# Kernel tuning notes

Measured on AMD Instinct MI355X. Metric: run time of the kernel, lower is better.

The kernel has to match this reference:

```python
import jax, jax.numpy as jnp
import numpy as np

D_MODEL = 1024
N_HEAD = 16


def setup_inputs() -> dict:
    key = jax.random.key(0)
    ks = jax.random.split(key, 12)
    B, T, D = 2, 2048, D_MODEL
    s = 1.0 / np.sqrt(D)
    return {
        "q": jax.random.normal(ks[0], (B, T, D), jnp.float32),
        "k": jax.random.normal(ks[1], (B, T, D), jnp.float32),
        "v": jax.random.normal(ks[2], (B, T, D), jnp.float32),
        "w_q": jax.random.normal(ks[3], (D, D), jnp.float32) * s,
        "b_q": jnp.zeros((D,), jnp.float32),
        "w_k": jax.random.normal(ks[4], (D, D), jnp.float32) * s,
        "b_k": jnp.zeros((D,), jnp.float32),
        "w_v": jax.random.normal(ks[5], (D, D), jnp.float32) * s,
        "b_v": jnp.zeros((D,), jnp.float32),
        "w_o": jax.random.normal(ks[6], (D, D), jnp.float32) * s,
        "b_o": jnp.zeros((D,), jnp.float32),
    }


def reference(q, k, v, w_q, b_q, w_k, b_k, w_v, b_v, w_o, b_o):
    B, T, D = q.shape
    H = N_HEAD
    nd = D // H  # head dim
    # projections (weights stored as [in, out])
    qh = (q @ w_q + b_q).reshape(B, T, H, nd).transpose(0, 2, 1, 3)  # [b,h,t,nd]
    kh = (k @ w_k + b_k).reshape(B, T, H, nd).transpose(0, 2, 1, 3)
    vh = (v @ w_v + b_v).reshape(B, T, H, nd).transpose(0, 2, 1, 3)
    score = jnp.einsum('bhqd,bhkd->bhqk', qh, kh) / jnp.sqrt(jnp.float32(nd))
    causal = jnp.tril(jnp.ones((T, T), dtype=bool))  # [tq, tk]
    score = jnp.where(causal, score, -jnp.inf)
    # NOTE: original module uses nn.Softmax(dim=-2), i.e. softmax over the
    # QUERY axis. Faithful to the source.
    attn = jax.nn.softmax(score, axis=-2)
    out = jnp.einsum('bhqk,bhkd->bhqd', attn, vh)  # [b,h,t,nd]
    out = out.transpose(0, 2, 1, 3).reshape(B, T, D)
    return out @ w_o + b_o
```

## Files before the change

### kernel.cpp

```cpp
#include <hip/hip_runtime.h>
#include <hip/hip_bf16.h>
#include <cstdint>
#include <cstddef>

#define D_MODEL 1024
#define NHEAD   16
#define HDIM    64
#define BB      2
#define TT      2048
#define MM      (BB*TT)
#define BHN     (BB*NHEAD)

typedef __attribute__((ext_vector_type(8))) __bf16 bf16x8;
typedef __attribute__((ext_vector_type(4))) float  f32x4;
typedef __attribute__((ext_vector_type(8))) unsigned short u16x8;
typedef __attribute__((ext_vector_type(4))) unsigned short u16x4;

__device__ __forceinline__ unsigned short f2b(float f){
  __bf16 b = (__bf16)f;
  return __builtin_bit_cast(unsigned short, b);
}

__device__ __forceinline__ f32x4 mfma16(bf16x8 a, bf16x8 b, f32x4 c){
  return __builtin_amdgcn_mfma_f32_16x16x32_bf16(a, b, c, 0, 0, 0);
}

__device__ __forceinline__ void gload16(const void* g, void* lds){
  __builtin_amdgcn_global_load_lds((const __attribute__((address_space(1))) void*)g,
                                   (__attribute__((address_space(3))) void*)lds, 16, 0, 0);
}

#define SWZ(byteoff, row) ((byteoff) ^ (((row)&7)<<4))

__global__ void cvt_bf16_kernel(const float* __restrict__ q, const float* __restrict__ k,
                                const float* __restrict__ v,
                                unsigned short* __restrict__ Xq, unsigned short* __restrict__ Xk,
                                unsigned short* __restrict__ Xv){
  const int z = blockIdx.y;
  const float* x = z==0 ? q : z==1 ? k : v;
  unsigned short* y = z==0 ? Xq : z==1 ? Xk : Xv;
  size_t i = (size_t)blockIdx.x*blockDim.x + threadIdx.x;
  const float4* p = (const float4*)(x + i*8);
  float4 a = p[0], b = p[1];
  u16x8 o;
  o[0]=f2b(a.x); o[1]=f2b(a.y); o[2]=f2b(a.z); o[3]=f2b(a.w);
  o[4]=f2b(b.x); o[5]=f2b(b.y); o[6]=f2b(b.z); o[7]=f2b(b.w);
  *(u16x8*)(y + i*8) = o;
}

__global__ void transpose_w_kernel(const float* __restrict__ W0, const float* __restrict__ W1,
                                   const float* __restrict__ W2, const float* __restrict__ W3,
                                   unsigned short* __restrict__ T0, unsigned short* __restrict__ T1,
                                   unsigned short* __restrict__ T2, unsigned short* __restrict__ T3){
  __shared__ float tile[32][33];
  const int z = blockIdx.z;
  const float* W = z==0 ? W0 : z==1 ? W1 : z==2 ? W2 : W3;
  unsigned short* Wt = z==0 ? T0 : z==1 ? T1 : z==2 ? T2 : T3;
  int tx = threadIdx.x, ty = threadIdx.y;
  int x0 = blockIdx.x*32, y0 = blockIdx.y*32;
  #pragma unroll
  for (int i=0;i<4;i++)
    tile[ty + i*8][tx] = W[(size_t)(y0 + ty + i*8)*D_MODEL + x0 + tx];
  __syncthreads();
  #pragma unroll
  for (int i=0;i<4;i++)
    Wt[(size_t)(x0 + ty + i*8)*D_MODEL + y0 + tx] = f2b(tile[tx][ty + i*8]);
}

__device__ __forceinline__ void gemm_body(const unsigned short* __restrict__ A,
                                          const unsigned short* __restrict__ Bt,
                                          const float* __restrict__ bias,
                                          void* __restrict__ Cout, const int mode,
                                          const int m0, const int n0)
{
  constexpr int K = D_MODEL, N = D_MODEL;
  __shared__ unsigned short As[128*64];
  __shared__ unsigned short Bs[128*64];
  const int t = threadIdx.x, lane = t&63, w = t>>6;
  const int wr = w>>1, wc = w&1, lr = lane&15, lg = lane>>4;
  const int osrc = (lane&7) ^ (lane>>3);
  f32x4 acc[4][4] = {};
  for (int k0 = 0; k0 < K; k0 += 64){
    __syncthreads();
    #pragma unroll
    for (int g=0; g<4; g++){
      int reg = w*4 + g;
      int r = reg*8 + (lane>>3);
      gload16(A  + (size_t)(m0+r)*K + k0 + osrc*8, (char*)As + reg*1024);
      gload16(Bt + (size_t)(n0+r)*K + k0 + osrc*8, (char*)Bs + reg*1024);
    }
    __syncthreads();
    #pragma unroll
    for (int ks=0; ks<2; ks++){
      bf16x8 af[4], bfv[4];
      #pragma unroll
      for (int mi=0;mi<4;mi++){
        int r = wr*64 + mi*16 + lr;
        af[mi] = *(const bf16x8*)((const char*)As + r*128 + (((ks*4+lg) ^ (r&7))*16));
      }
      #pragma unroll
      for (int ni=0;ni<4;ni++){
        int r = wc*64 + ni*16 + lr;
        bfv[ni] = *(const bf16x8*)((const char*)Bs + r*128 + (((ks*4+lg) ^ (r&7))*16));
      }
      #pragma unroll
      for (int mi=0;mi<4;mi++)
        #pragma unroll
        for (int ni=0;ni<4;ni++)
          acc[mi][ni] = mfma16(af[mi], bfv[ni], acc[mi][ni]);
    }
  }
  #pragma unroll
  for (int mi=0;mi<4;mi++){
    #pragma unroll
    for (int ni=0;ni<4;ni++){
      int n = n0 + wc*64 + ni*16 + lr;
      int mbase = m0 + wr*64 + mi*16 + lg*4;
      float bv = bias[n];
      if (mode == 2){
        float* Cf = (float*)Cout;
        #pragma unroll
        for (int r=0;r<4;r++) Cf[(size_t)(mbase+r)*N + n] = acc[mi][ni][r] + bv;
      } else if (mode == 0){
        unsigned short* Cb = (unsigned short*)Cout;
        #pragma unroll
        for (int r=0;r<4;r++) Cb[(size_t)(mbase+r)*N + n] = f2b(acc[mi][ni][r] + bv);
      } else {
        unsigned short* Vt = (unsigned short*)Cout;
        int h = n >> 6, d = n & 63;
        int b = mbase >> 11;
        int tq = mbase & (TT-1);
        u16x4 vv;
        #pragma unroll
        for (int r=0;r<4;r++) vv[r] = f2b(acc[mi][ni][r] + bv);
        *(u16x4*)(Vt + ((size_t)((b*NHEAD + h)*HDIM + d))*TT + tq) = vv;
      }
    }
  }
}

__launch_bounds__(256)
__global__ void proj_gemm_kernel(const unsigned short* __restrict__ Xq,
                                 const unsigned short* __restrict__ Xk,
                                 const unsigned short* __restrict__ Xv,
                                 const unsigned short* __restrict__ Wtq,
                                 const unsigned short* __restrict__ Wtk,
                                 const unsigned short* __restrict__ Wtv,
                                 const float* __restrict__ b_q, const float* __restrict__ b_k,
                                 const float* __restrict__ b_v,
                                 unsigned short* __restrict__ Qb, unsigned short* __restrict__ Kb,
                                 unsigned short* __restrict__ Vt)
{
  const int id = blockIdx.x;
  const int xcd = id & 7, r2 = id >> 3;
  const int n = r2 & 7, mz = r2 >> 3;
  const int m = (mz & 3)*8 + xcd, z = mz >> 2;
  const unsigned short* A  = z==0 ? Xq : z==1 ? Xk : Xv;
  const unsigned short* Bt = z==0 ? Wtq : z==1 ? Wtk : Wtv;
  const float* bias = z==0 ? b_q : z==1 ? b_k : b_v;
  void* C = z==0 ? (void*)Qb : z==1 ? (void*)Kb : (void*)Vt;
  gemm_body(A, Bt, bias, C, z==2 ? 1 : 0, m*128, n*128);
}

__launch_bounds__(256)
__global__ void out_gemm_kernel(const unsigned short* __restrict__ Ob,
                                const unsigned short* __restrict__ Wto,
                                const float* __restrict__ b_o, float* __restrict__ out)
{
  const int id = blockIdx.x;
  const int xcd = id & 7, r2 = id >> 3;
  const int n = r2 & 7, m = (r2 >> 3)*8 + xcd;
  gemm_body(Ob, Wto, b_o, out, 2, m*128, n*128);
}

__launch_bounds__(256)
__global__ void col_stats_kernel(const unsigned short* __restrict__ Qb,
                                 const unsigned short* __restrict__ Kb,
                                 float* __restrict__ partialS)
{
  __shared__ unsigned short Ks[128*64];
  __shared__ unsigned short Qs[64*64];
  const int t = threadIdx.x, lane = t&63, w = t>>6;
  const int id = blockIdx.x;
  const int bh = id & 31, pair = id >> 5;
  const int kb_ = pair & 15, qc = pair >> 4;
  const int b = bh >> 4, h = bh & 15;
  const int k0 = kb_ * 128;
  const int lr = lane&15, lg = lane>>4;
  #pragma unroll
  for (int i=0;i<4;i++){
    int c = i*256 + t; int r = c>>3, o = c&7;
    uint4 vv = *(const uint4*)(Kb + ((size_t)(b*TT + k0 + r))*D_MODEL + h*64 + o*8);
    *(uint4*)((char*)Ks + SWZ(r*128 + o*16, r)) = vv;
  }
  __syncthreads();
  bf16x8 bk[2][2];
  #pragma unroll
  for (int kb=0;kb<2;kb++)
    #pragma unroll
    for (int ks=0;ks<2;ks++){
      int r = w*32 + kb*16 + lr;
      bk[kb][ks] = *(const bf16x8*)((const char*)Ks + SWZ(r*128 + ks*64 + lg*16, r));
    }
  f32x4 sacc[2] = {};
  const int qstart = (k0 > qc*256) ? k0 : qc*256;
  const int qend   = (qc+1)*256;
  for (int qt = qstart; qt < qend; qt += 64){
    __syncthreads();
    #pragma unroll
    for (int i=0;i<2;i++){
      int c = i*256 + t; int r = c>>3, o = c&7;
      uint4 vv = *(const uint4*)(Qb + ((size_t)(b*TT + qt + r))*D_MODEL + h*64 + o*8);
      *(uint4*)((char*)Qs + SWZ(r*128 + o*16, r)) = vv;
    }
    __syncthreads();
    const bool interior = (qt >= k0 + 128);
    #pragma unroll
    for (int qb=0;qb<4;qb++){
      bf16x8 aq[2];
      #pragma unroll
      for (int ks=0;ks<2;ks++){
        int r = qb*16 + lr;
        aq[ks] = *(const bf16x8*)((const char*)Qs + SWZ(r*128 + ks*64 + lg*16, r));
      }
      f32x4 sf[2] = {};
      #pragma unroll
      for (int ks=0;ks<2;ks++)
        #pragma unroll
        for (int kb=0;kb<2;kb++)
          sf[kb] = mfma16(aq[ks], bk[kb][ks], sf[kb]);
      #pragma unroll
      for (int kb=0;kb<2;kb++){
        int col = k0 + w*32 + kb*16 + lr;
        #pragma unroll
        for (int r=0;r<4;r++){
          float e = __expf(sf[kb][r] * 0.125f);
          if (!interior){
            int qg = qt + qb*16 + lg*4 + r;
            e = (qg >= col) ? e : 0.f;
          }
          sacc[kb][r] += e;
        }
      }
    }
  }
  #pragma unroll
  for (int kb=0;kb<2;kb++){
    float s = sacc[kb][0] + sacc[kb][1] + sacc[kb][2] + sacc[kb][3];
    s += __shfl_xor(s, 16);
    s += __shfl_xor(s, 32);
    if (lg == 0){
      int col = k0 + w*32 + kb*16 + lr;
      partialS[((size_t)qc*BHN + bh)*TT + col] = s;
    }
  }
}

__global__ void col_combine_kernel(const float* __restrict__ partialS, float* __restrict__ colS){
  int i = blockIdx.x*256 + threadIdx.x;
  float s = 0.f;
  #pragma unroll
  for (int qc=0;qc<8;qc++) s += partialS[(size_t)qc*BHN*TT + i];
  colS[i] = 1.0f / s;
}

__launch_bounds__(256)
__global__ void attn_out_kernel(const unsigned short* __restrict__ Qb,
                                const unsigned short* __restrict__ Kb,
                                const unsigned short* __restrict__ Vt,
                                const float* __restrict__ colS,
                                unsigned short* __restrict__ O)
{
  __shared__ unsigned short Qs[64*64];
  __shared__ unsigned short Ks2[64*64];
  __shared__ unsigned short Vs[64*64];
  __shared__ unsigned short Ps[64*64];
  const int t = threadIdx.x, lane=t&63, w=t>>6;
  const int id = blockIdx.x;
  const int bh = id & 31;
  const int qi = 31 - (id >> 5);
  const int b = bh>>4, h = bh&15;
  const int q0 = qi*64;
  const int lr = lane&15, lg = lane>>4;
  #pragma unroll
  for (int i=0;i<2;i++){
    int c = i*256+t; int r=c>>3, o=c&7;
    uint4 vv = *(const uint4*)(Qb + ((size_t)(b*TT + q0 + r))*D_MODEL + h*64 + o*8);
    *(uint4*)((char*)Qs + SWZ(r*128 + o*16, r)) = vv;
  }
  __syncthreads();
  bf16x8 aq[2];
  #pragma unroll
  for (int ks=0;ks<2;ks++){
    int r = w*16 + lr;
    aq[ks] = *(const bf16x8*)((const char*)Qs + SWZ(r*128 + ks*64 + lg*16, r));
  }
  f32x4 oacc[4] = {};
  const int nkt = qi + 1;
  for (int kt=0; kt<nkt; kt++){
    int k0 = kt*64;
    __syncthreads();
    #pragma unroll
    for (int i=0;i<2;i++){
      int c = i*256+t; int r=c>>3, o=c&7;
      uint4 vk = *(const uint4*)(Kb + ((size_t)(b*TT + k0 + r))*D_MODEL + h*64 + o*8);
      uint4 vv = *(const uint4*)(Vt + ((size_t)(bh*HDIM + r))*TT + k0 + o*8);
      int byte = SWZ(r*128 + o*16, r);
      *(uint4*)((char*)Ks2 + byte) = vk;
      *(uint4*)((char*)Vs  + byte) = vv;
    }
    __syncthreads();
    f32x4 sf[4] = {};
    #pragma unroll
    for (int ks=0;ks<2;ks++)
      #pragma unroll
      for (int kb=0;kb<4;kb++){
        int r = kb*16 + lr;
        bf16x8 bk = *(const bf16x8*)((const char*)Ks2 + SWZ(r*128 + ks*64 + lg*16, r));
        sf[kb] = mfma16(aq[ks], bk, sf[kb]);
      }
    const bool boundary = (kt == qi);
    #pragma unroll
    for (int kb=0;kb<4;kb++){
      int col = k0 + kb*16 + lr;
      float isc = colS[(size_t)bh*TT + col];
      #pragma unroll
      for (int r=0;r<4;r++){
        int prow = w*16 + lg*4 + r;
        float pv = __expf(sf[kb][r]*0.125f) * isc;
        if (boundary){
          int qg = q0 + prow;
          pv = (qg >= col) ? pv : 0.f;
        }
        *(unsigned short*)((char*)Ps + SWZ((prow*64 + kb*16 + lr)*2, prow)) = f2b(pv);
      }
    }
    #pragma unroll
    for (int ks=0;ks<2;ks++){
      int pr = w*16 + lr;
      bf16x8 pa = *(const bf16x8*)((const char*)Ps + SWZ(pr*128 + ks*64 + lg*16, pr));
      #pragma unroll
      for (int db=0;db<4;db++){
        int r = db*16 + lr;
        bf16x8 bv = *(const bf16x8*)((const char*)Vs + SWZ(r*128 + ks*64 + lg*16, r));
        oacc[db] = mfma16(pa, bv, oacc[db]);
      }
    }
  }
  #pragma unroll
  for (int db=0;db<4;db++){
    int qg = q0 + w*16 + lg*4;
    int d  = db*16 + lr;
    #pragma unroll
    for (int r=0;r<4;r++)
      O[((size_t)(b*TT + qg + r))*D_MODEL + h*64 + d] = f2b(oacc[db][r]);
  }
}

extern "C" void kernel_launch(void* const* d_in, const int* in_sizes, int n_in,
                              void* d_out, int out_size, void* d_ws, size_t ws_size,
                              hipStream_t stream)
{
  (void)in_sizes; (void)n_in; (void)out_size; (void)ws_size;
  const float* q   = (const float*)d_in[0];
  const float* k   = (const float*)d_in[1];
  const float* v   = (const float*)d_in[2];
  const float* w_q = (const float*)d_in[3];
  const float* b_q = (const float*)d_in[4];
  const float* w_k = (const float*)d_in[5];
  const float* b_k = (const float*)d_in[6];
  const float* w_v = (const float*)d_in[7];
  const float* b_v = (const float*)d_in[8];
  const float* w_o = (const float*)d_in[9];
  const float* b_o = (const float*)d_in[10];

  char* p = (char*)d_ws;
  auto carve = [&](size_t bytes)->char* {
    char* r = p; p += (bytes + 255) & ~(size_t)255; return r;
  };
  unsigned short* Xq  = (unsigned short*)carve((size_t)MM*D_MODEL*2);
  unsigned short* Xk  = (unsigned short*)carve((size_t)MM*D_MODEL*2);
  unsigned short* Xv  = (unsigned short*)carve((size_t)MM*D_MODEL*2);
  unsigned short* Wtq = (unsigned short*)carve((size_t)D_MODEL*D_MODEL*2);
  unsigned short* Wtk = (unsigned short*)carve((size_t)D_MODEL*D_MODEL*2);
  unsigned short* Wtv = (unsigned short*)carve((size_t)D_MODEL*D_MODEL*2);
  unsigned short* Wto = (unsigned short*)carve((size_t)D_MODEL*D_MODEL*2);
  unsigned short* Qb  = (unsigned short*)carve((size_t)MM*D_MODEL*2);
  unsigned short* Kb  = (unsigned short*)carve((size_t)MM*D_MODEL*2);
  unsigned short* Vt  = (unsigned short*)carve((size_t)MM*D_MODEL*2);
  unsigned short* Ob  = (unsigned short*)carve((size_t)MM*D_MODEL*2);
  float* partialS = (float*)carve((size_t)8*BHN*TT*4);
  float* colS     = (float*)carve((size_t)BHN*TT*4);

  cvt_bf16_kernel<<<dim3((MM*D_MODEL/8)/256, 3), 256, 0, stream>>>(q, k, v, Xq, Xk, Xv);

  dim3 tgrid(32,32,4), tblk(32,8);
  transpose_w_kernel<<<tgrid, tblk, 0, stream>>>(w_q, w_k, w_v, w_o, Wtq, Wtk, Wtv, Wto);

  proj_gemm_kernel<<<dim3(768), 256, 0, stream>>>(Xq, Xk, Xv, Wtq, Wtk, Wtv,
                                                  b_q, b_k, b_v, Qb, Kb, Vt);

  col_stats_kernel<<<dim3(8*16*BHN), 256, 0, stream>>>(Qb, Kb, partialS);
  col_combine_kernel<<<dim3(BHN*TT/256), 256, 0, stream>>>(partialS, colS);

  attn_out_kernel<<<dim3((TT/64)*BHN), 256, 0, stream>>>(Qb, Kb, Vt, colS, Ob);

  out_gemm_kernel<<<dim3(256), 256, 0, stream>>>(Ob, Wto, b_o, (float*)d_out);
}
```

Baseline: 167.2 us.

## Use direct-to-LDS loads in attention, pre-scale V by column sums, retile output GEMM

Attention and column-stats kernels now stage K, Q and V tiles with global_load_lds and apply the XOR swizzle on the source side, replacing register round-trip copies. The per-column softmax normalizer is folded into V by a new vscale pass, so the attention kernel no longer loads colS or multiplies per element. The S MFMA is transposed so that P rows can be written as packed 4-element LDS stores instead of scalar stores. The output GEMM moves to a dedicated 64x128 tile kernel with twice as many blocks to raise parallelism. The cost is an extra read-modify-write pass over V and an extra bf16 rounding of the scaled V.

Result: faster. 143.9 us (-13.9%).

```diff
diff --git a/kernel.cpp b/kernel.cpp
--- a/kernel.cpp
+++ b/kernel.cpp
@@ -19,6 +19,10 @@
 __device__ __forceinline__ unsigned short f2b(float f){
   __bf16 b = (__bf16)f;
   return __builtin_bit_cast(unsigned short, b);
+}
+__device__ __forceinline__ float b2f(unsigned short u){
+  unsigned int x = ((unsigned int)u) << 16;
+  return __builtin_bit_cast(float, x);
 }
 
 __device__ __forceinline__ f32x4 mfma16(bf16x8 a, bf16x8 b, f32x4 c){
@@ -117,11 +121,7 @@
       int n = n0 + wc*64 + ni*16 + lr;
       int mbase = m0 + wr*64 + mi*16 + lg*4;
       float bv = bias[n];
-      if (mode == 2){
-        float* Cf = (float*)Cout;
-        #pragma unroll
-        for (int r=0;r<4;r++) Cf[(size_t)(mbase+r)*N + n] = acc[mi][ni][r] + bv;
-      } else if (mode == 0){
+      if (mode == 0){
         unsigned short* Cb = (unsigned short*)Cout;
         #pragma unroll
         for (int r=0;r<4;r++) Cb[(size_t)(mbase+r)*N + n] = f2b(acc[mi][ni][r] + bv);
@@ -167,10 +167,62 @@
                                 const unsigned short* __restrict__ Wto,
                                 const float* __restrict__ b_o, float* __restrict__ out)
 {
+  constexpr int K = D_MODEL, N = D_MODEL;
+  __shared__ unsigned short As[64*64];
+  __shared__ unsigned short Bs[128*64];
   const int id = blockIdx.x;
   const int xcd = id & 7, r2 = id >> 3;
-  const int n = r2 & 7, m = (r2 >> 3)*8 + xcd;
-  gemm_body(Ob, Wto, b_o, out, 2, m*128, n*128);
+  const int n0 = (r2 & 7)*128, m0 = ((r2 >> 3)*8 + xcd)*64;
+  const int t = threadIdx.x, lane = t&63, w = t>>6;
+  const int wr = w>>1, wc = w&1, lr = lane&15, lg = lane>>4;
+  const int osrc = (lane&7) ^ (lane>>3);
+  f32x4 acc[2][4] = {};
+  for (int k0 = 0; k0 < K; k0 += 64){
+    __syncthreads();
+    #pragma unroll
+    for (int g=0; g<2; g++){
+      int reg = w*2 + g;
+      int r = reg*8 + (lane>>3);
+      gload16(Ob + (size_t)(m0+r)*K + k0 + osrc*8, (char*)As + reg*1024);
+    }
+    #pragma unroll
+    for (int g=0; g<4; g++){
+      int reg = w*4 + g;
+      int r = reg*8 + (lane>>3);
+      gload16(Wto + (size_t)(n0+r)*K + k0 + osrc*8, (char*)Bs + reg*1024);
+    }
+    __syncthreads();
+    #pragma unroll
+    for (int ks=0; ks<2; ks++){
+      bf16x8 af[2], bfv[4];
+      #pragma unroll
+      for (int mi=0;mi<2;mi++){
+        int r = wr*32 + mi*16 + lr;
+        af[mi] = *(const bf16x8*)((const char*)As + r*128 + (((ks*4+lg) ^ (r&7))*16));
+      }
+      #pragma unroll
+      for (int ni=0;ni<4;ni++){
+        int r = wc*64 + ni*16 + lr;
+        bfv[ni] = *(const bf16x8*)((const char*)Bs + r*128 + (((ks*4+lg) ^ (r&7))*16));
+      }
+      #pragma unroll
+      for (int mi=0;mi<2;mi++)
+        #pragma unroll
+        for (int ni=0;ni<4;ni++)
+          acc[mi][ni] = mfma16(af[mi], bfv[ni], acc[mi][ni]);
+    }
+  }
+  #pragma unroll
+  for (int mi=0;mi<2;mi++){
+    #pragma unroll
+    for (int ni=0;ni<4;ni++){
+      int n = n0 + wc*64 + ni*16 + lr;
+      int mbase = m0 + wr*32 + mi*16 + lg*4;
+      float bv = b_o[n];
+      #pragma unroll
+      for (int r=0;r<4;r++) out[(size_t)(mbase+r)*N + n] = acc[mi][ni][r] + bv;
+    }
+  }
 }
 
 __launch_bounds__(256)
@@ -187,11 +239,12 @@
   const int b = bh >> 4, h = bh & 15;
   const int k0 = kb_ * 128;
   const int lr = lane&15, lg = lane>>4;
-  #pragma unroll
-  for (int i=0;i<4;i++){
-    int c = i*256 + t; int r = c>>3, o = c&7;
-    uint4 vv = *(const uint4*)(Kb + ((size_t)(b*TT + k0 + r))*D_MODEL + h*64 + o*8);
-    *(uint4*)((char*)Ks + SWZ(r*128 + o*16, r)) = vv;
+  const int osrc = (lane&7) ^ (lane>>3);
+  #pragma unroll
+  for (int g=0; g<4; g++){
+    int reg = w*4 + g;
+    int r = reg*8 + (lane>>3);
+    gload16(Kb + ((size_t)(b*TT + k0 + r))*D_MODEL + h*64 + osrc*8, (char*)Ks + reg*1024);
   }
   __syncthreads();
   bf16x8 bk[2][2];
@@ -200,7 +253,7 @@
     #pragma unroll
     for (int ks=0;ks<2;ks++){
       int r = w*32 + kb*16 + lr;
-      bk[kb][ks] = *(const bf16x8*)((const char*)Ks + SWZ(r*128 + ks*64 + lg*16, r));
+      bk[kb][ks] = *(const bf16x8*)((const char*)Ks + r*128 + (((ks*4+lg) ^ (r&7))*16));
     }
   f32x4 sacc[2] = {};
   const int qstart = (k0 > qc*256) ? k0 : qc*256;
@@ -208,10 +261,10 @@
   for (int qt = qstart; qt < qend; qt += 64){
     __syncthreads();
     #pragma unroll
-    for (int i=0;i<2;i++){
-      int c = i*256 + t; int r = c>>3, o = c&7;
-      uint4 vv = *(const uint4*)(Qb + ((size_t)(b*TT + qt + r))*D_MODEL + h*64 + o*8);
-      *(uint4*)((char*)Qs + SWZ(r*128 + o*16, r)) = vv;
+    for (int g=0; g<2; g++){
+      int reg = w*2 + g;
+      int r = reg*8 + (lane>>3);
+      gload16(Qb + ((size_t)(b*TT + qt + r))*D_MODEL + h*64 + osrc*8, (char*)Qs + reg*1024);
     }
     __syncthreads();
     const bool interior = (qt >= k0 + 128);
@@ -221,7 +274,7 @@
       #pragma unroll
       for (int ks=0;ks<2;ks++){
         int r = qb*16 + lr;
-        aq[ks] = *(const bf16x8*)((const char*)Qs + SWZ(r*128 + ks*64 + lg*16, r));
+        aq[ks] = *(const bf16x8*)((const char*)Qs + r*128 + (((ks*4+lg) ^ (r&7))*16));
       }
       f32x4 sf[2] = {};
       #pragma unroll
@@ -264,11 +317,25 @@
   colS[i] = 1.0f / s;
 }
 
+__global__ void vscale_kernel(unsigned short* __restrict__ Vt, const float* __restrict__ colS){
+  size_t c = (size_t)blockIdx.x*256 + threadIdx.x;
+  int t0  = (int)(c & 255) * 8;
+  int row = (int)(c >> 8);
+  int bh  = row >> 6;
+  u16x8 v = *(u16x8*)(Vt + (size_t)row*TT + t0);
+  const float4* cs = (const float4*)(colS + (size_t)bh*TT + t0);
+  float4 s0 = cs[0], s1 = cs[1];
+  v[0]=f2b(b2f(v[0])*s0.x); v[1]=f2b(b2f(v[1])*s0.y);
+  v[2]=f2b(b2f(v[2])*s0.z); v[3]=f2b(b2f(v[3])*s0.w);
+  v[4]=f2b(b2f(v[4])*s1.x); v[5]=f2b(b2f(v[5])*s1.y);
+  v[6]=f2b(b2f(v[6])*s1.z); v[7]=f2b(b2f(v[7])*s1.w);
+  *(u16x8*)(Vt + (size_t)row*TT + t0) = v;
+}
+
 __launch_bounds__(256)
 __global__ void attn_out_kernel(const unsigned short* __restrict__ Qb,
                                 const unsigned short* __restrict__ Kb,
                                 const unsigned short* __restrict__ Vt,
-                                const float* __restrict__ colS,
                                 unsigned short* __restrict__ O)
 {
   __shared__ unsigned short Qs[64*64];
@@ -282,18 +349,19 @@
   const int b = bh>>4, h = bh&15;
   const int q0 = qi*64;
   const int lr = lane&15, lg = lane>>4;
-  #pragma unroll
-  for (int i=0;i<2;i++){
-    int c = i*256+t; int r=c>>3, o=c&7;
-    uint4 vv = *(const uint4*)(Qb + ((size_t)(b*TT + q0 + r))*D_MODEL + h*64 + o*8);
-    *(uint4*)((char*)Qs + SWZ(r*128 + o*16, r)) = vv;
+  const int osrc = (lane&7) ^ (lane>>3);
+  #pragma unroll
+  for (int g=0; g<2; g++){
+    int reg = w*2 + g;
+    int r = reg*8 + (lane>>3);
+    gload16(Qb + ((size_t)(b*TT + q0 + r))*D_MODEL + h*64 + osrc*8, (char*)Qs + reg*1024);
   }
   __syncthreads();
   bf16x8 aq[2];
   #pragma unroll
   for (int ks=0;ks<2;ks++){
     int r = w*16 + lr;
-    aq[ks] = *(const bf16x8*)((const char*)Qs + SWZ(r*128 + ks*64 + lg*16, r));
+    aq[ks] = *(const bf16x8*)((const char*)Qs + r*128 + (((ks*4+lg) ^ (r&7))*16));
   }
   f32x4 oacc[4] = {};
   const int nkt = qi + 1;
@@ -301,13 +369,11 @@
     int k0 = kt*64;
     __syncthreads();
     #pragma unroll
-    for (int i=0;i<2;i++){
-      int c = i*256+t; int r=c>>3, o=c&7;
-      uint4 vk = *(const uint4*)(Kb + ((size_t)(b*TT + k0 + r))*D_MODEL + h*64 + o*8);
-      uint4 vv = *(const uint4*)(Vt + ((size_t)(bh*HDIM + r))*TT + k0 + o*8);
-      int byte = SWZ(r*128 + o*16, r);
-      *(uint4*)((char*)Ks2 + byte) = vk;
-      *(uint4*)((char*)Vs  + byte) = vv;
+    for (int g=0; g<2; g++){
+      int reg = w*2 + g;
+      int r = reg*8 + (lane>>3);
+      gload16(Kb + ((size_t)(b*TT + k0 + r))*D_MODEL + h*64 + osrc*8, (char*)Ks2 + reg*1024);
+      gload16(Vt + ((size_t)(bh*HDIM + r))*TT + k0 + osrc*8, (char*)Vs + reg*1024);
     }
     __syncthreads();
     f32x4 sf[4] = {};
@@ -316,33 +382,33 @@
       #pragma unroll
       for (int kb=0;kb<4;kb++){
         int r = kb*16 + lr;
-        bf16x8 bk = *(const bf16x8*)((const char*)Ks2 + SWZ(r*128 + ks*64 + lg*16, r));
-        sf[kb] = mfma16(aq[ks], bk, sf[kb]);
+        bf16x8 bk = *(const bf16x8*)((const char*)Ks2 + r*128 + (((ks*4+lg) ^ (r&7))*16));
+        sf[kb] = mfma16(bk, aq[ks], sf[kb]);
       }
     const bool boundary = (kt == qi);
+    const int prow = w*16 + lr;
     #pragma unroll
     for (int kb=0;kb<4;kb++){
-      int col = k0 + kb*16 + lr;
-      float isc = colS[(size_t)bh*TT + col];
+      u16x4 vv;
       #pragma unroll
       for (int r=0;r<4;r++){
-        int prow = w*16 + lg*4 + r;
-        float pv = __expf(sf[kb][r]*0.125f) * isc;
+        float pv = __expf(sf[kb][r]*0.125f);
         if (boundary){
+          int kg = k0 + kb*16 + lg*4 + r;
           int qg = q0 + prow;
-          pv = (qg >= col) ? pv : 0.f;
+          pv = (qg >= kg) ? pv : 0.f;
         }
-        *(unsigned short*)((char*)Ps + SWZ((prow*64 + kb*16 + lr)*2, prow)) = f2b(pv);
-      }
+        vv[r] = f2b(pv);
+      }
+      *(u16x4*)((char*)Ps + SWZ(prow*128 + kb*32 + lg*8, prow)) = vv;
     }
     #pragma unroll
     for (int ks=0;ks<2;ks++){
-      int pr = w*16 + lr;
-      bf16x8 pa = *(const bf16x8*)((const char*)Ps + SWZ(pr*128 + ks*64 + lg*16, pr));
+      bf16x8 pa = *(const bf16x8*)((const char*)Ps + prow*128 + (((ks*4+lg) ^ (prow&7))*16));
       #pragma unroll
       for (int db=0;db<4;db++){
         int r = db*16 + lr;
-        bf16x8 bv = *(const bf16x8*)((const char*)Vs + SWZ(r*128 + ks*64 + lg*16, r));
+        bf16x8 bv = *(const bf16x8*)((const char*)Vs + r*128 + (((ks*4+lg) ^ (r&7))*16));
         oacc[db] = mfma16(pa, bv, oacc[db]);
       }
     }
@@ -403,7 +469,9 @@
   col_stats_kernel<<<dim3(8*16*BHN), 256, 0, stream>>>(Qb, Kb, partialS);
   col_combine_kernel<<<dim3(BHN*TT/256), 256, 0, stream>>>(partialS, colS);
 
-  attn_out_kernel<<<dim3((TT/64)*BHN), 256, 0, stream>>>(Qb, Kb, Vt, colS, Ob);
-
-  out_gemm_kernel<<<dim3(256), 256, 0, stream>>>(Ob, Wto, b_o, (float*)d_out);
-}
+  vscale_kernel<<<dim3((BHN*HDIM*TT/8)/256), 256, 0, stream>>>(Vt, colS);
+
+  attn_out_kernel<<<dim3((TT/64)*BHN), 256, 0, stream>>>(Qb, Kb, Vt, Ob);
+
+  out_gemm_kernel<<<dim3(512), 256, 0, stream>>>(Ob, Wto, b_o, (float*)d_out);
+}
```
